# Kernel optimization log

Hardware: AMD Instinct MI355X
Metric: run time of the kernel (lower is better)

Reference implementation:

```python
import jax, jax.numpy as jnp
import numpy as np

B, S, H = 1, 1024, 2048
NH, NKV, HD = 16, 4, 128          # attention heads, kv heads, head_dim
NKUV, E, F = 4, 8, 256            # ffn kuv heads, experts, experts_dim
TOPK = 2
EPS = 1e-6
SCALE = HD ** -0.5


def setup_inputs():
    key = jax.random.key(0)
    ks = jax.random.split(key, 10)
    rn = lambda k, shp, s=0.02: jax.random.normal(k, shp, jnp.float32) * s
    hidden_states = jax.random.normal(ks[0], (B, S, H), jnp.float32)
    # real RoPE tables (base 10000)
    inv = 1.0 / (10000.0 ** (jnp.arange(0, HD, 2, dtype=jnp.float32) / HD))
    freqs = jnp.arange(S, dtype=jnp.float32)[:, None] * inv[None, :]
    emb = jnp.concatenate([freqs, freqs], axis=-1)          # (S, HD)
    cos = jnp.broadcast_to(jnp.cos(emb), (B, S, HD))
    sin = jnp.broadcast_to(jnp.sin(emb), (B, S, HD))
    # additive causal mask
    causal = jnp.tril(jnp.ones((S, S), bool))
    attn_mask = jnp.where(causal, 0.0, -1e9).astype(jnp.float32)[None, None]
    return dict(
        hidden_states=hidden_states, cos=cos, sin=sin, attn_mask=attn_mask,
        ln1_w=jnp.ones((H,), jnp.float32), ln2_w=jnp.ones((H,), jnp.float32),
        wq=rn(ks[1], (NH * HD, H)), wk=rn(ks[2], (NKV * HD, H)),
        wv=rn(ks[3], (NKV * HD, H)), wo=rn(ks[4], (H, NH * HD)),
        mh_norm_w=jnp.ones((NH, HD), jnp.float32),
        router_w=rn(ks[5], (NH, E, HD)),
        k_w=rn(ks[6], (NKUV, E, F, HD)), u_w=rn(ks[7], (NKUV, E, F, HD)),
        v_w=rn(ks[8], (NKUV, E, F, HD)),
    )


def _rmsnorm(x, w, eps=EPS):
    xf = x.astype(jnp.float32)
    var = jnp.mean(xf * xf, axis=-1, keepdims=True)
    return (xf * jax.lax.rsqrt(var + eps) * w).astype(x.dtype)


def _rotate_half(x):
    x1, x2 = jnp.split(x, 2, axis=-1)
    return jnp.concatenate([-x2, x1], axis=-1)


def reference(hidden_states, cos, sin, attn_mask, ln1_w, ln2_w,
              wq, wk, wv, wo, mh_norm_w, router_w, k_w, u_w, v_w):
    # ---- attention block (pre-norm + GQA + RoPE) ----
    x = _rmsnorm(hidden_states, ln1_w)
    q = (x @ wq.T).reshape(B, S, NH, HD).transpose(0, 2, 1, 3)    # (B,NH,S,HD)
    k = (x @ wk.T).reshape(B, S, NKV, HD).transpose(0, 2, 1, 3)   # (B,NKV,S,HD)
    v = (x @ wv.T).reshape(B, S, NKV, HD).transpose(0, 2, 1, 3)
    c, s = cos[:, None], sin[:, None]                              # unsqueeze_dim=1
    q = q * c + _rotate_half(q) * s
    k = k * c + _rotate_half(k) * s
    rep = NH // NKV
    k = jnp.repeat(k, rep, axis=1)                                 # repeat_kv
    v = jnp.repeat(v, rep, axis=1)
    scores = jnp.einsum('bhqd,bhkd->bhqk', q, k) * SCALE + attn_mask
    probs = jax.nn.softmax(scores.astype(jnp.float32), axis=-1).astype(q.dtype)
    attn = jnp.einsum('bhqk,bhkd->bqhd', probs, v).reshape(B, S, NH * HD)
    h = hidden_states + attn @ wo.T
    # ---- multi-head MoE FFN block ----
    y = _rmsnorm(h, ln2_w).reshape(B, S, NH, HD)
    y = _rmsnorm(y, mh_norm_w)                                     # per-head norm
    logits = jnp.einsum('bsnd,ned->bsne', y, router_w)
    rp = jax.nn.softmax(logits.astype(jnp.float32), axis=-1)
    topv, topi = jax.lax.top_k(rp, TOPK)                           # (B,S,NH,TOPK)
    topv = topv / jnp.sum(topv, axis=-1, keepdims=True)
    w_dense = jnp.sum(jax.nn.one_hot(topi, E, dtype=jnp.float32) * topv[..., None],
                      axis=-2).astype(y.dtype)                     # (B,S,NH,E)
    reph = NH // NKUV
    kf = jnp.repeat(k_w, reph, axis=0)                             # repeat_kuv -> (NH,E,F,HD)
    uf = jnp.repeat(u_w, reph, axis=0)
    vf = jnp.repeat(v_w, reph, axis=0)
    gate = jnp.einsum('bsnd,nefd->bsnef', y, kf)
    up = jnp.einsum('bsnd,nefd->bsnef', y, uf)
    act = jax.nn.silu(gate) * up * w_dense[..., None]              # sparse combine weights
    ffn = jnp.einsum('bsnef,nefd->bsnd', act, vf).reshape(B, S, H)
    return h + ffn
```

## Files before the change

### kernel.cpp

```cpp
#include <hip/hip_runtime.h>
#include <hip/hip_bf16.h>

#define S_ 1024
#define H_ 2048
#define NH_ 16
#define NKV_ 4
#define HD_ 128
#define E_ 8
#define F_ 256
#define EPS_ 1e-6f
#define SCALE_ 0.08838834764831845f

typedef __attribute__((ext_vector_type(8))) short bf16x8;
typedef __attribute__((ext_vector_type(4))) float f32x4;

static __device__ __forceinline__ unsigned short f2bf(float x) {
  unsigned u = __float_as_uint(x);
  unsigned r = (u + 0x7FFFu + ((u >> 16) & 1u)) >> 16;
  return (unsigned short)r;
}
static __device__ __forceinline__ float bf2f(unsigned short b) {
  return __uint_as_float(((unsigned)b) << 16);
}
static __device__ __forceinline__ unsigned short f2bh(float x) {
  __hip_bfloat16 b = __float2bfloat16(x);
  return *reinterpret_cast<unsigned short*>(&b);
}

__global__ void rmsnorm1_kernel(const float* __restrict__ in, const float* __restrict__ w,
                                float* __restrict__ out) {
  int s = blockIdx.x, tid = threadIdx.x;
  const float* row = in + s * H_;
  __shared__ float red[256];
  float ss = 0.f;
  for (int i = tid; i < H_; i += 256) { float v = row[i]; ss += v * v; }
  red[tid] = ss; __syncthreads();
  for (int off = 128; off > 0; off >>= 1) {
    if (tid < off) red[tid] += red[tid + off];
    __syncthreads();
  }
  float rs = rsqrtf(red[0] / H_ + EPS_);
  for (int i = tid; i < H_; i += 256) out[s * H_ + i] = row[i] * rs * w[i];
}

__global__ __launch_bounds__(256) void convert_kuw_kernel(const float* __restrict__ kw,
                                                          const float* __restrict__ uw,
                                                          unsigned short* __restrict__ kwb,
                                                          unsigned short* __restrict__ uwb) {
  const float* src = (blockIdx.y == 0) ? kw : uw;
  unsigned short* dst = (blockIdx.y == 0) ? kwb : uwb;
  size_t i = ((size_t)blockIdx.x * 256 + threadIdx.x) * 8;
  float4 a = *(const float4*)&src[i];
  float4 b = *(const float4*)&src[i + 4];
  ushort4 ua, ub;
  ua.x = f2bh(a.x); ua.y = f2bh(a.y); ua.z = f2bh(a.z); ua.w = f2bh(a.w);
  ub.x = f2bh(b.x); ub.y = f2bh(b.y); ub.z = f2bh(b.z); ub.w = f2bh(b.w);
  *(ushort4*)&dst[i] = ua;
  *(ushort4*)&dst[i + 4] = ub;
}

__global__ __launch_bounds__(256) void transpose_vw_kernel(const float* __restrict__ vw,
                                                           unsigned short* __restrict__ vwtb) {
  int e = blockIdx.x, ft = blockIdx.y, dt = blockIdx.z;
  int tid = threadIdx.x;
  __shared__ float tile[64][65];
  const float* src = vw + ((size_t)e * 256 + ft * 64) * 128 + dt * 64;
#pragma unroll
  for (int it = 0; it < 4; ++it) {
    int idx = it * 256 + tid;
    int r = idx >> 4, c4 = (idx & 15) * 4;
    float4 v = *(const float4*)&src[(size_t)r * 128 + c4];
    tile[r][c4] = v.x; tile[r][c4 + 1] = v.y; tile[r][c4 + 2] = v.z; tile[r][c4 + 3] = v.w;
  }
  __syncthreads();
  unsigned short* dst = vwtb + ((size_t)e * 128 + dt * 64) * 256 + ft * 64;
#pragma unroll
  for (int it = 0; it < 4; ++it) {
    int idx = it * 256 + tid;
    int dl = idx >> 4, f4 = (idx & 15) * 4;
    ushort4 u;
    u.x = f2bh(tile[f4 + 0][dl]); u.y = f2bh(tile[f4 + 1][dl]);
    u.z = f2bh(tile[f4 + 2][dl]); u.w = f2bh(tile[f4 + 3][dl]);
    *(ushort4*)&dst[(size_t)dl * 256 + f4] = u;
  }
}

__global__ __launch_bounds__(256) void qkv_mfma_kernel(const float* __restrict__ A,
                                                       const float* __restrict__ wq,
                                                       const float* __restrict__ wk,
                                                       const float* __restrict__ wv,
                                                       float* __restrict__ qb,
                                                       float* __restrict__ kb,
                                                       float* __restrict__ vb) {
  int bm = blockIdx.y * 128;
  int bn = blockIdx.x * 128;
  const float* B; float* C; int ldc, cb;
  if (bn < 2048)      { B = wq + (size_t)bn * 2048;          C = qb; ldc = 2048; cb = bn; }
  else if (bn < 2560) { B = wk + (size_t)(bn - 2048) * 2048; C = kb; ldc = 512;  cb = bn - 2048; }
  else                { B = wv + (size_t)(bn - 2560) * 2048; C = vb; ldc = 512;  cb = bn - 2560; }
  int tid = threadIdx.x, wave = tid >> 6, lane = tid & 63;
  int lq = lane & 15, lg4 = lane >> 4;
  int wr = (wave >> 1) * 64, wc = (wave & 1) * 64;
  __shared__ __align__(16) unsigned short Als[128 * 64];
  __shared__ __align__(16) unsigned short Bls[128 * 64];
  f32x4 acc[4][4];
#pragma unroll
  for (int i = 0; i < 4; ++i)
#pragma unroll
    for (int j = 0; j < 4; ++j) acc[i][j] = (f32x4){0.f, 0.f, 0.f, 0.f};
  for (int k0 = 0; k0 < 2048; k0 += 64) {
    __syncthreads();
#pragma unroll
    for (int it = 0; it < 8; ++it) {
      int idx = it * 256 + tid;
      int r = idx >> 4, c4 = (idx & 15) * 4;
      float4 av = *(const float4*)&A[(size_t)(bm + r) * 2048 + k0 + c4];
      ushort4 ua; ua.x = f2bh(av.x); ua.y = f2bh(av.y); ua.z = f2bh(av.z); ua.w = f2bh(av.w);
      *(ushort4*)((char*)Als + ((r * 128 + c4 * 2) ^ ((r & 7) << 4))) = ua;
      float4 bv = *(const float4*)&B[(size_t)r * 2048 + k0 + c4];
      ushort4 ub; ub.x = f2bh(bv.x); ub.y = f2bh(bv.y); ub.z = f2bh(bv.z); ub.w = f2bh(bv.w);
      *(ushort4*)((char*)Bls + ((r * 128 + c4 * 2) ^ ((r & 7) << 4))) = ub;
    }
    __syncthreads();
#pragma unroll
    for (int ks = 0; ks < 2; ++ks) {
      bf16x8 af[4], bfr[4];
#pragma unroll
      for (int mi = 0; mi < 4; ++mi) {
        int row = wr + mi * 16 + lq;
        af[mi] = *(const bf16x8*)((const char*)Als + ((row * 128 + ks * 64 + lg4 * 16) ^ ((row & 7) << 4)));
      }
#pragma unroll
      for (int ni = 0; ni < 4; ++ni) {
        int row = wc + ni * 16 + lq;
        bfr[ni] = *(const bf16x8*)((const char*)Bls + ((row * 128 + ks * 64 + lg4 * 16) ^ ((row & 7) << 4)));
      }
#pragma unroll
      for (int mi = 0; mi < 4; ++mi)
#pragma unroll
        for (int ni = 0; ni < 4; ++ni)
          acc[mi][ni] = __builtin_amdgcn_mfma_f32_16x16x32_bf16(af[mi], bfr[ni], acc[mi][ni], 0, 0, 0);
    }
  }
#pragma unroll
  for (int mi = 0; mi < 4; ++mi)
#pragma unroll
    for (int ni = 0; ni < 4; ++ni) {
      int col = cb + wc + ni * 16 + lq;
#pragma unroll
      for (int reg = 0; reg < 4; ++reg) {
        int m = bm + wr + mi * 16 + lg4 * 4 + reg;
        C[(size_t)m * ldc + col] = acc[mi][ni][reg];
      }
    }
}

__global__ __launch_bounds__(256) void wo_mfma_kernel(const float* __restrict__ A,
                                                      const float* __restrict__ Bmat,
                                                      const float* __restrict__ resid,
                                                      float* __restrict__ C) {
  int bm = blockIdx.y * 128;
  int bn = blockIdx.x * 128;
  int tid = threadIdx.x, wave = tid >> 6, lane = tid & 63;
  int lq = lane & 15, lg4 = lane >> 4;
  int wr = (wave >> 1) * 64, wc = (wave & 1) * 64;
  __shared__ __align__(16) unsigned short Als[128 * 64];
  __shared__ __align__(16) unsigned short Bls[128 * 64];
  f32x4 acc[4][4];
#pragma unroll
  for (int i = 0; i < 4; ++i)
#pragma unroll
    for (int j = 0; j < 4; ++j) acc[i][j] = (f32x4){0.f, 0.f, 0.f, 0.f};
  for (int k0 = 0; k0 < 2048; k0 += 64) {
    __syncthreads();
#pragma unroll
    for (int it = 0; it < 8; ++it) {
      int idx = it * 256 + tid;
      int r = idx >> 4, c4 = (idx & 15) * 4;
      float4 av = *(const float4*)&A[(size_t)(bm + r) * 2048 + k0 + c4];
      ushort4 ua; ua.x = f2bh(av.x); ua.y = f2bh(av.y); ua.z = f2bh(av.z); ua.w = f2bh(av.w);
      *(ushort4*)((char*)Als + ((r * 128 + c4 * 2) ^ ((r & 7) << 4))) = ua;
      float4 bv = *(const float4*)&Bmat[(size_t)(bn + r) * 2048 + k0 + c4];
      ushort4 ub; ub.x = f2bh(bv.x); ub.y = f2bh(bv.y); ub.z = f2bh(bv.z); ub.w = f2bh(bv.w);
      *(ushort4*)((char*)Bls + ((r * 128 + c4 * 2) ^ ((r & 7) << 4))) = ub;
    }
    __syncthreads();
#pragma unroll
    for (int ks = 0; ks < 2; ++ks) {
      bf16x8 af[4], bfr[4];
#pragma unroll
      for (int mi = 0; mi < 4; ++mi) {
        int row = wr + mi * 16 + lq;
        af[mi] = *(const bf16x8*)((const char*)Als + ((row * 128 + ks * 64 + lg4 * 16) ^ ((row & 7) << 4)));
      }
#pragma unroll
      for (int ni = 0; ni < 4; ++ni) {
        int row = wc + ni * 16 + lq;
        bfr[ni] = *(const bf16x8*)((const char*)Bls + ((row * 128 + ks * 64 + lg4 * 16) ^ ((row & 7) << 4)));
      }
#pragma unroll
      for (int mi = 0; mi < 4; ++mi)
#pragma unroll
        for (int ni = 0; ni < 4; ++ni)
          acc[mi][ni] = __builtin_amdgcn_mfma_f32_16x16x32_bf16(af[mi], bfr[ni], acc[mi][ni], 0, 0, 0);
    }
  }
#pragma unroll
  for (int mi = 0; mi < 4; ++mi)
#pragma unroll
    for (int ni = 0; ni < 4; ++ni) {
      int col = bn + wc + ni * 16 + lq;
#pragma unroll
      for (int reg = 0; reg < 4; ++reg) {
        int m = bm + wr + mi * 16 + lg4 * 4 + reg;
        C[(size_t)m * 2048 + col] = acc[mi][ni][reg] + resid[(size_t)m * 2048 + col];
      }
    }
}

__global__ void rope_kernel(float* __restrict__ qb, float* __restrict__ kb,
                            const float* __restrict__ cosb, const float* __restrict__ sinb) {
  int s = blockIdx.x, tid = threadIdx.x;
  for (int idx = tid; idx < (NH_ + NKV_) * 64; idx += 256) {
    int hh = idx >> 6;
    int d = idx & 63;
    float c0 = cosb[s * HD_ + d], s0 = sinb[s * HD_ + d];
    float c1 = cosb[s * HD_ + d + 64], s1 = sinb[s * HD_ + d + 64];
    float* p;
    if (hh < NH_) p = qb + (size_t)s * 2048 + hh * 128;
    else          p = kb + (size_t)s * 512 + (hh - NH_) * 128;
    float a = p[d], b = p[d + 64];
    p[d] = a * c0 - b * s0;
    p[d + 64] = b * c1 + a * s1;
  }
}

__global__ __launch_bounds__(256) void attn_mfma_kernel(const float* __restrict__ qb,
                                                        const float* __restrict__ kb,
                                                        const float* __restrict__ vb,
                                                        float* __restrict__ ob) {
  int n = blockIdx.x, qt = blockIdx.y;
  int g = n >> 2;
  int tid = threadIdx.x;
  int wave = tid >> 6, lane = tid & 63;
  int lq = lane & 15, lg4 = lane >> 4;

  __shared__ __align__(16) unsigned short Kls[64 * 128];
  __shared__ __align__(16) unsigned short Vls[128 * 64];
  __shared__ __align__(16) unsigned short Pls[4][16 * 64];
  __shared__ __align__(16) float corr_ls[4][16];
  __shared__ __align__(16) float lsum_ls[4][16];

  int q0 = qt * 64 + wave * 16;
  bf16x8 qfrag[4];
  {
    const float* qp = qb + (size_t)(q0 + lq) * 2048 + n * 128;
#pragma unroll
    for (int ks = 0; ks < 4; ++ks) {
      float4 a = *(const float4*)&qp[ks * 32 + lg4 * 8];
      float4 b = *(const float4*)&qp[ks * 32 + lg4 * 8 + 4];
      bf16x8 f;
      f[0] = (short)f2bf(a.x); f[1] = (short)f2bf(a.y);
      f[2] = (short)f2bf(a.z); f[3] = (short)f2bf(a.w);
      f[4] = (short)f2bf(b.x); f[5] = (short)f2bf(b.y);
      f[6] = (short)f2bf(b.z); f[7] = (short)f2bf(b.w);
      qfrag[ks] = f;
    }
  }
  f32x4 oacc[8];
#pragma unroll
  for (int i = 0; i < 8; ++i) oacc[i] = (f32x4){0.f, 0.f, 0.f, 0.f};
  float mrow = -1e30f, lrow = 0.f;

  int nt = qt + 1;
  for (int t = 0; t < nt; ++t) {
    int kv0 = t * 64;
    __syncthreads();
#pragma unroll
    for (int it = 0; it < 8; ++it) {
      int idx = it * 256 + tid;
      int r = idx >> 5;
      int c4 = (idx & 31) * 4;
      size_t gbase = (size_t)(kv0 + r) * 512 + g * 128 + c4;
      float4 kv = *(const float4*)&kb[gbase];
      ushort4 u;
      u.x = f2bf(kv.x); u.y = f2bf(kv.y); u.z = f2bf(kv.z); u.w = f2bf(kv.w);
      *(ushort4*)((char*)Kls + ((r * 256 + c4 * 2) ^ ((r & 7) << 4))) = u;
      float4 vv = *(const float4*)&vb[gbase];
      unsigned short vs0 = f2bf(vv.x), vs1 = f2bf(vv.y), vs2 = f2bf(vv.z), vs3 = f2bf(vv.w);
      *(unsigned short*)((char*)Vls + (((c4 + 0) * 128 + r * 2) ^ (((c4 + 0) & 7) << 4))) = vs0;
      *(unsigned short*)((char*)Vls + (((c4 + 1) * 128 + r * 2) ^ (((c4 + 1) & 7) << 4))) = vs1;
      *(unsigned short*)((char*)Vls + (((c4 + 2) * 128 + r * 2) ^ (((c4 + 2) & 7) << 4))) = vs2;
      *(unsigned short*)((char*)Vls + (((c4 + 3) * 128 + r * 2) ^ (((c4 + 3) & 7) << 4))) = vs3;
    }
    __syncthreads();
    f32x4 sacc[4];
#pragma unroll
    for (int i = 0; i < 4; ++i) sacc[i] = (f32x4){0.f, 0.f, 0.f, 0.f};
#pragma unroll
    for (int kt = 0; kt < 4; ++kt) {
      int row = kt * 16 + lq;
#pragma unroll
      for (int ks = 0; ks < 4; ++ks) {
        bf16x8 kf = *(const bf16x8*)((const char*)Kls +
                     ((row * 256 + ks * 64 + lg4 * 16) ^ ((row & 7) << 4)));
        sacc[kt] = __builtin_amdgcn_mfma_f32_16x16x32_bf16(kf, qfrag[ks], sacc[kt], 0, 0, 0);
      }
    }
    int qg = q0 + lq;
    float s[16], p[16];
    float rmax = -1e30f;
#pragma unroll
    for (int kt = 0; kt < 4; ++kt) {
#pragma unroll
      for (int r = 0; r < 4; ++r) {
        int kg = kv0 + kt * 16 + lg4 * 4 + r;
        float v = sacc[kt][r] * SCALE_;
        v = (kg <= qg) ? v : -1e30f;
        s[kt * 4 + r] = v;
        rmax = fmaxf(rmax, v);
      }
    }
    rmax = fmaxf(rmax, __shfl_xor(rmax, 16));
    rmax = fmaxf(rmax, __shfl_xor(rmax, 32));
    float mnew = fmaxf(mrow, rmax);
    float corr = __expf(mrow - mnew);
    float psum = 0.f;
#pragma unroll
    for (int i = 0; i < 16; ++i) { p[i] = __expf(s[i] - mnew); psum += p[i]; }
    psum += __shfl_xor(psum, 16);
    psum += __shfl_xor(psum, 32);
    lrow = lrow * corr + psum;
    mrow = mnew;
    if (lane < 16) corr_ls[wave][lq] = corr;
#pragma unroll
    for (int kt = 0; kt < 4; ++kt) {
      unsigned u0 = (unsigned)f2bf(p[kt * 4 + 0]) | ((unsigned)f2bf(p[kt * 4 + 1]) << 16);
      unsigned u1 = (unsigned)f2bf(p[kt * 4 + 2]) | ((unsigned)f2bf(p[kt * 4 + 3]) << 16);
      int colb = kt * 32 + lg4 * 8;
      *(unsigned*)((char*)&Pls[wave][0] + ((lq * 128 + colb) ^ ((lq & 7) << 4))) = u0;
      *(unsigned*)((char*)&Pls[wave][0] + ((lq * 128 + colb + 4) ^ ((lq & 7) << 4))) = u1;
    }
    f32x4 c4v = *(const f32x4*)&corr_ls[wave][lg4 * 4];
#pragma unroll
    for (int dt = 0; dt < 8; ++dt) {
#pragma unroll
      for (int r = 0; r < 4; ++r) oacc[dt][r] *= c4v[r];
    }
    bf16x8 pfrag[2];
#pragma unroll
    for (int ks2 = 0; ks2 < 2; ++ks2)
      pfrag[ks2] = *(const bf16x8*)((const char*)&Pls[wave][0] +
                    ((lq * 128 + ks2 * 64 + lg4 * 16) ^ ((lq & 7) << 4)));
#pragma unroll
    for (int dt = 0; dt < 8; ++dt) {
      int dr = dt * 16 + lq;
#pragma unroll
      for (int ks2 = 0; ks2 < 2; ++ks2) {
        bf16x8 vf = *(const bf16x8*)((const char*)Vls +
                     ((dr * 128 + ks2 * 64 + lg4 * 16) ^ ((dr & 7) << 4)));
        oacc[dt] = __builtin_amdgcn_mfma_f32_16x16x32_bf16(pfrag[ks2], vf, oacc[dt], 0, 0, 0);
      }
    }
  }
  if (lane < 16) lsum_ls[wave][lq] = lrow;
  f32x4 l4 = *(const f32x4*)&lsum_ls[wave][lg4 * 4];
#pragma unroll
  for (int dt = 0; dt < 8; ++dt) {
#pragma unroll
    for (int r = 0; r < 4; ++r) {
      ob[(size_t)(q0 + lg4 * 4 + r) * 2048 + n * 128 + dt * 16 + lq] = oacc[dt][r] / l4[r];
    }
  }
}

__global__ void rmsnorm2_kernel(const float* __restrict__ hin, const float* __restrict__ ln2w,
                                const float* __restrict__ mhw, float* __restrict__ yout,
                                unsigned short* __restrict__ ybb) {
  int s = blockIdx.x, tid = threadIdx.x;
  const float* row = hin + (size_t)s * H_;
  __shared__ float y1[H_];
  __shared__ float red[256];
  __shared__ float ph[16][17];
  float ss = 0.f;
  for (int i = tid; i < H_; i += 256) { float v = row[i]; ss += v * v; }
  red[tid] = ss; __syncthreads();
  for (int off = 128; off > 0; off >>= 1) {
    if (tid < off) red[tid] += red[tid + off];
    __syncthreads();
  }
  float rs1 = rsqrtf(red[0] / H_ + EPS_);
  for (int i = tid; i < H_; i += 256) y1[i] = row[i] * rs1 * ln2w[i];
  __syncthreads();
  int n = tid >> 4, j = tid & 15;
  float s2 = 0.f;
  for (int d = j * 8; d < j * 8 + 8; ++d) { float v = y1[n * 128 + d]; s2 += v * v; }
  ph[n][j] = s2; __syncthreads();
  if (j == 0) {
    float t = 0.f;
    for (int q = 0; q < 16; ++q) t += ph[n][q];
    ph[n][16] = rsqrtf(t / HD_ + EPS_);
  }
  __syncthreads();
  for (int i = tid; i < H_; i += 256) {
    int hn = i >> 7;
    float v = y1[i] * ph[hn][16] * mhw[i];
    yout[(size_t)s * H_ + i] = v;
    ybb[(size_t)s * H_ + i] = f2bh(v);
  }
}

__global__ void route_kernel(const float* __restrict__ yb, const float* __restrict__ rw,
                             int* __restrict__ cnt, int* __restrict__ idxb,
                             float* __restrict__ wtb) {
  int s = blockIdx.x, tid = threadIdx.x;
  int n = tid >> 3, e = tid & 7;
  const float* yrow = yb + (size_t)s * 2048 + n * 128;
  const float* wrow = rw + (size_t)(n * 8 + e) * 128;
  float lg = 0.f;
  for (int d = 0; d < 128; ++d) lg += yrow[d] * wrow[d];
  float mx = lg;
  for (int off = 1; off < 8; off <<= 1) mx = fmaxf(mx, __shfl_xor(mx, off));
  float p = __expf(lg - mx);
  float sum = p;
  for (int off = 1; off < 8; off <<= 1) sum += __shfl_xor(sum, off);
  float rp = p / sum;
  float v1 = rp; int i1 = e;
  for (int off = 1; off < 8; off <<= 1) {
    float ov = __shfl_xor(v1, off); int oi = __shfl_xor(i1, off);
    if (ov > v1 || (ov == v1 && oi < i1)) { v1 = ov; i1 = oi; }
  }
  float v2 = (e == i1) ? -1e30f : rp; int i2 = e;
  for (int off = 1; off < 8; off <<= 1) {
    float ov = __shfl_xor(v2, off); int oi = __shfl_xor(i2, off);
    if (ov > v2 || (ov == v2 && oi < i2)) { v2 = ov; i2 = oi; }
  }
  if (e == 0) {
    float wsum = v1 + v2;
    int pe1 = n * 8 + i1;
    int pos1 = atomicAdd(&cnt[pe1], 1);
    idxb[pe1 * S_ + pos1] = s; wtb[pe1 * S_ + pos1] = v1 / wsum;
    int pe2 = n * 8 + i2;
    int pos2 = atomicAdd(&cnt[pe2], 1);
    idxb[pe2 * S_ + pos2] = s; wtb[pe2 * S_ + pos2] = v2 / wsum;
  }
}

__global__ __launch_bounds__(256) void moe_ffn_mfma_kernel(
    const unsigned short* __restrict__ ybb, const unsigned short* __restrict__ kwb,
    const unsigned short* __restrict__ uwb, const unsigned short* __restrict__ vwtb,
    const int* __restrict__ cnt, const int* __restrict__ idxb,
    const float* __restrict__ wtb, float* __restrict__ out) {
  int pe = blockIdx.x;
  int c = cnt[pe];
  int base = blockIdx.y * 64;
  if (base >= c) return;
  int n = pe >> 3, e = pe & 7, g = n >> 2;
  int eW = g * 8 + e;
  int nr = min(64, c - base);
  int tid = threadIdx.x, wave = tid >> 6, lane = tid & 63;
  int lq = lane & 15, lg4 = lane >> 4;

  __shared__ __align__(16) unsigned short Yls[64 * 128];
  __shared__ __align__(16) unsigned short WstK[64 * 128];
  __shared__ __align__(16) unsigned short WstU[64 * 128];
  __shared__ __align__(16) unsigned short WstV[128 * 64];
  __shared__ __align__(16) unsigned short Act[4][16 * 64];
  __shared__ int sidx[64];
  __shared__ float swt[64];

  if (tid < 64) {
    sidx[tid] = (tid < nr) ? idxb[pe * S_ + base + tid] : 0;
    swt[tid]  = (tid < nr) ? wtb[pe * S_ + base + tid] : 0.f;
  }
  __syncthreads();
#pragma unroll
  for (int it = 0; it < 4; ++it) {
    int idx = it * 256 + tid;
    int r = idx >> 4, c8 = (idx & 15) * 8;
    bf16x8 v = {0, 0, 0, 0, 0, 0, 0, 0};
    if (r < nr) v = *(const bf16x8*)&ybb[(size_t)sidx[r] * 2048 + n * 128 + c8];
    *(bf16x8*)((char*)Yls + ((r * 256 + c8 * 2) ^ ((r & 7) << 4))) = v;
  }
  __syncthreads();
  bf16x8 yfrag[4];
  {
    int arow = wave * 16 + lq;
#pragma unroll
    for (int ks = 0; ks < 4; ++ks)
      yfrag[ks] = *(const bf16x8*)((const char*)Yls + ((arow * 256 + ks * 64 + lg4 * 16) ^ ((arow & 7) << 4)));
  }
  float wts[4];
#pragma unroll
  for (int reg = 0; reg < 4; ++reg) wts[reg] = swt[wave * 16 + lg4 * 4 + reg];

  f32x4 dacc[8];
#pragma unroll
  for (int i = 0; i < 8; ++i) dacc[i] = (f32x4){0.f, 0.f, 0.f, 0.f};

  for (int fc = 0; fc < 4; ++fc) {
    __syncthreads();
#pragma unroll
    for (int it = 0; it < 4; ++it) {
      int idx = it * 256 + tid;
      int r = idx >> 4, c8 = (idx & 15) * 8;
      size_t goff = ((size_t)(eW * 256 + fc * 64 + r)) * 128 + c8;
      bf16x8 kv = *(const bf16x8*)&kwb[goff];
      *(bf16x8*)((char*)WstK + ((r * 256 + c8 * 2) ^ ((r & 7) << 4))) = kv;
      bf16x8 uv = *(const bf16x8*)&uwb[goff];
      *(bf16x8*)((char*)WstU + ((r * 256 + c8 * 2) ^ ((r & 7) << 4))) = uv;
    }
#pragma unroll
    for (int it = 0; it < 4; ++it) {
      int idx = it * 256 + tid;
      int r = idx >> 3, c8 = (idx & 7) * 8;
      bf16x8 vv = *(const bf16x8*)&vwtb[((size_t)(eW * 128 + r)) * 256 + fc * 64 + c8];
      *(bf16x8*)((char*)WstV + ((r * 128 + c8 * 2) ^ ((r & 7) << 4))) = vv;
    }
    __syncthreads();
    f32x4 gacc[4], uacc[4];
#pragma unroll
    for (int i = 0; i < 4; ++i) { gacc[i] = (f32x4){0.f, 0.f, 0.f, 0.f}; uacc[i] = (f32x4){0.f, 0.f, 0.f, 0.f}; }
#pragma unroll
    for (int ks = 0; ks < 4; ++ks) {
#pragma unroll
      for (int nf = 0; nf < 4; ++nf) {
        int brow = nf * 16 + lq;
        bf16x8 bk = *(const bf16x8*)((const char*)WstK + ((brow * 256 + ks * 64 + lg4 * 16) ^ ((brow & 7) << 4)));
        gacc[nf] = __builtin_amdgcn_mfma_f32_16x16x32_bf16(yfrag[ks], bk, gacc[nf], 0, 0, 0);
        bf16x8 bu = *(const bf16x8*)((const char*)WstU + ((brow * 256 + ks * 64 + lg4 * 16) ^ ((brow & 7) << 4)));
        uacc[nf] = __builtin_amdgcn_mfma_f32_16x16x32_bf16(yfrag[ks], bu, uacc[nf], 0, 0, 0);
      }
    }
#pragma unroll
    for (int nf = 0; nf < 4; ++nf) {
#pragma unroll
      for (int reg = 0; reg < 4; ++reg) {
        int m = lg4 * 4 + reg;
        int f = nf * 16 + lq;
        float gg = gacc[nf][reg];
        float uu = uacc[nf][reg];
        float sig = 1.f / (1.f + __expf(-gg));
        float av = gg * sig * uu * wts[reg];
        *(unsigned short*)((char*)&Act[wave][0] + ((m * 128 + f * 2) ^ ((m & 7) << 4))) = f2bh(av);
      }
    }
    bf16x8 afrag[2];
#pragma unroll
    for (int ks2 = 0; ks2 < 2; ++ks2)
      afrag[ks2] = *(const bf16x8*)((const char*)&Act[wave][0] + ((lq * 128 + ks2 * 64 + lg4 * 16) ^ ((lq & 7) << 4)));
#pragma unroll
    for (int nd = 0; nd < 8; ++nd) {
      int drow = nd * 16 + lq;
#pragma unroll
      for (int ks2 = 0; ks2 < 2; ++ks2) {
        bf16x8 b = *(const bf16x8*)((const char*)WstV + ((drow * 128 + ks2 * 64 + lg4 * 16) ^ ((drow & 7) << 4)));
        dacc[nd] = __builtin_amdgcn_mfma_f32_16x16x32_bf16(afrag[ks2], b, dacc[nd], 0, 0, 0);
      }
    }
  }
#pragma unroll
  for (int nd = 0; nd < 8; ++nd) {
    int d = nd * 16 + lq;
#pragma unroll
    for (int reg = 0; reg < 4; ++reg) {
      int mloc = wave * 16 + lg4 * 4 + reg;
      if (mloc < nr) {
        atomicAdd(&out[(size_t)sidx[mloc] * 2048 + n * 128 + d], dacc[nd][reg]);
      }
    }
  }
}

extern "C" void kernel_launch(void* const* d_in, const int* in_sizes, int n_in,
                              void* d_out, int out_size, void* d_ws, size_t ws_size,
                              hipStream_t stream) {
  const float* hidden = (const float*)d_in[0];
  const float* cosb   = (const float*)d_in[1];
  const float* sinb   = (const float*)d_in[2];
  const float* ln1w   = (const float*)d_in[4];
  const float* ln2w   = (const float*)d_in[5];
  const float* wq     = (const float*)d_in[6];
  const float* wk     = (const float*)d_in[7];
  const float* wv     = (const float*)d_in[8];
  const float* wo     = (const float*)d_in[9];
  const float* mhw    = (const float*)d_in[10];
  const float* rw     = (const float*)d_in[11];
  const float* kww    = (const float*)d_in[12];
  const float* uww    = (const float*)d_in[13];
  const float* vww    = (const float*)d_in[14];
  float* out = (float*)d_out;

  float* ws = (float*)d_ws;
  float* x     = ws;
  float* qb    = x + 2097152;
  float* kb    = qb + 2097152;
  float* vb    = kb + 524288;
  float* attnb = vb + 524288;
  float* yb    = attnb + 2097152;
  int*   cntb  = (int*)(yb + 2097152);
  int*   idxb  = cntb + 128;
  float* wtb   = (float*)(idxb + 131072);
  unsigned short* ybb  = (unsigned short*)(wtb + 131072);
  unsigned short* kwb  = ybb + 2097152;
  unsigned short* uwb  = kwb + 1048576;
  unsigned short* vwtb = uwb + 1048576;

  hipMemsetAsync(cntb, 0, 128 * sizeof(int), stream);

  convert_kuw_kernel<<<dim3(512, 2), 256, 0, stream>>>(kww, uww, kwb, uwb);
  transpose_vw_kernel<<<dim3(32, 4, 2), 256, 0, stream>>>(vww, vwtb);

  rmsnorm1_kernel<<<S_, 256, 0, stream>>>(hidden, ln1w, x);

  qkv_mfma_kernel<<<dim3(24, 8), 256, 0, stream>>>(x, wq, wk, wv, qb, kb, vb);

  rope_kernel<<<S_, 256, 0, stream>>>(qb, kb, cosb, sinb);

  attn_mfma_kernel<<<dim3(NH_, S_ / 64), 256, 0, stream>>>(qb, kb, vb, attnb);

  wo_mfma_kernel<<<dim3(16, 8), 256, 0, stream>>>(attnb, wo, hidden, out);

  rmsnorm2_kernel<<<S_, 256, 0, stream>>>(out, ln2w, mhw, yb, ybb);

  route_kernel<<<S_, 128, 0, stream>>>(yb, rw, cntb, idxb, wtb);

  moe_ffn_mfma_kernel<<<dim3(128, 16), 256, 0, stream>>>(ybb, kwb, uwb, vwtb, cntb, idxb, wtb, out);
}
```

Baseline: 437.7 us.

## Store intermediates in bf16 and double-buffer QKV/WO GEMMs with smaller tiles

The normalized input, V, the roped Q/K and the attention output are now written as bf16 instead of fp32, which halves their memory traffic and removes repeated conversions in the consumer kernels. The QKV and output-projection GEMMs switch to 64x128 tiles with a swizzled 1D grid, so more blocks run and neighbouring blocks share data in cache. They also use a register-staged double buffer that overlaps global loads with MFMA work. The attention K/V staging uses wider 16-byte loads. Rounding happens earlier in the pipeline, though operands were already converted to bf16 before the MFMAs.

```diff
diff --git a/kernel.cpp b/kernel.cpp
--- a/kernel.cpp
+++ b/kernel.cpp
@@ -19,16 +19,13 @@
   unsigned r = (u + 0x7FFFu + ((u >> 16) & 1u)) >> 16;
   return (unsigned short)r;
 }
-static __device__ __forceinline__ float bf2f(unsigned short b) {
-  return __uint_as_float(((unsigned)b) << 16);
-}
 static __device__ __forceinline__ unsigned short f2bh(float x) {
   __hip_bfloat16 b = __float2bfloat16(x);
   return *reinterpret_cast<unsigned short*>(&b);
 }
 
 __global__ void rmsnorm1_kernel(const float* __restrict__ in, const float* __restrict__ w,
-                                float* __restrict__ out) {
+                                unsigned short* __restrict__ outb) {
   int s = blockIdx.x, tid = threadIdx.x;
   const float* row = in + s * H_;
   __shared__ float red[256];
@@ -40,7 +37,7 @@
     __syncthreads();
   }
   float rs = rsqrtf(red[0] / H_ + EPS_);
-  for (int i = tid; i < H_; i += 256) out[s * H_ + i] = row[i] * rs * w[i];
+  for (int i = tid; i < H_; i += 256) outb[(size_t)s * H_ + i] = f2bh(row[i] * rs * w[i]);
 }
 
 __global__ __launch_bounds__(256) void convert_kuw_kernel(const float* __restrict__ kw,
@@ -85,128 +82,179 @@
   }
 }
 
-__global__ __launch_bounds__(256) void qkv_mfma_kernel(const float* __restrict__ A,
+__global__ __launch_bounds__(256) void qkv_mfma_kernel(const unsigned short* __restrict__ xb,
                                                        const float* __restrict__ wq,
                                                        const float* __restrict__ wk,
                                                        const float* __restrict__ wv,
                                                        float* __restrict__ qb,
                                                        float* __restrict__ kb,
-                                                       float* __restrict__ vb) {
-  int bm = blockIdx.y * 128;
-  int bn = blockIdx.x * 128;
-  const float* B; float* C; int ldc, cb;
+                                                       unsigned short* __restrict__ vbb) {
+  int bid = blockIdx.x;
+  int swz = (bid & 7) * 48 + (bid >> 3);
+  int bm = (swz / 24) * 64;
+  int bn = (swz % 24) * 128;
+  const float* B; float* C = nullptr; unsigned short* Cb = nullptr; int ldc, cb;
   if (bn < 2048)      { B = wq + (size_t)bn * 2048;          C = qb; ldc = 2048; cb = bn; }
   else if (bn < 2560) { B = wk + (size_t)(bn - 2048) * 2048; C = kb; ldc = 512;  cb = bn - 2048; }
-  else                { B = wv + (size_t)(bn - 2560) * 2048; C = vb; ldc = 512;  cb = bn - 2560; }
+  else                { B = wv + (size_t)(bn - 2560) * 2048; Cb = vbb; ldc = 512; cb = bn - 2560; }
   int tid = threadIdx.x, wave = tid >> 6, lane = tid & 63;
   int lq = lane & 15, lg4 = lane >> 4;
-  int wr = (wave >> 1) * 64, wc = (wave & 1) * 64;
-  __shared__ __align__(16) unsigned short Als[128 * 64];
-  __shared__ __align__(16) unsigned short Bls[128 * 64];
-  f32x4 acc[4][4];
-#pragma unroll
-  for (int i = 0; i < 4; ++i)
+  int wr = (wave >> 1) * 32, wc = (wave & 1) * 64;
+  __shared__ __align__(16) unsigned short Als[2][64 * 64];
+  __shared__ __align__(16) unsigned short Bls[2][128 * 64];
+  f32x4 acc[2][4];
+#pragma unroll
+  for (int i = 0; i < 2; ++i)
 #pragma unroll
     for (int j = 0; j < 4; ++j) acc[i][j] = (f32x4){0.f, 0.f, 0.f, 0.f};
-  for (int k0 = 0; k0 < 2048; k0 += 64) {
-    __syncthreads();
+
+  int ar = (tid >> 3), ac8 = (tid & 7) * 8;
+  int br = (tid >> 4), bc4 = (tid & 15) * 4;
+  bf16x8 areg[2];
+  float4 breg[8];
+
+  auto LOAD = [&](int k0) {
+#pragma unroll
+    for (int it = 0; it < 2; ++it)
+      areg[it] = *(const bf16x8*)&xb[(size_t)(bm + ar + it * 32) * 2048 + k0 + ac8];
+#pragma unroll
+    for (int it = 0; it < 8; ++it)
+      breg[it] = *(const float4*)&B[(size_t)(br + it * 16) * 2048 + k0 + bc4];
+  };
+  auto STORE = [&](int buf) {
+#pragma unroll
+    for (int it = 0; it < 2; ++it) {
+      int r = ar + it * 32;
+      *(bf16x8*)((char*)&Als[buf][0] + ((r * 128 + ac8 * 2) ^ ((r & 7) << 4))) = areg[it];
+    }
 #pragma unroll
     for (int it = 0; it < 8; ++it) {
-      int idx = it * 256 + tid;
-      int r = idx >> 4, c4 = (idx & 15) * 4;
-      float4 av = *(const float4*)&A[(size_t)(bm + r) * 2048 + k0 + c4];
-      ushort4 ua; ua.x = f2bh(av.x); ua.y = f2bh(av.y); ua.z = f2bh(av.z); ua.w = f2bh(av.w);
-      *(ushort4*)((char*)Als + ((r * 128 + c4 * 2) ^ ((r & 7) << 4))) = ua;
-      float4 bv = *(const float4*)&B[(size_t)r * 2048 + k0 + c4];
-      ushort4 ub; ub.x = f2bh(bv.x); ub.y = f2bh(bv.y); ub.z = f2bh(bv.z); ub.w = f2bh(bv.w);
-      *(ushort4*)((char*)Bls + ((r * 128 + c4 * 2) ^ ((r & 7) << 4))) = ub;
-    }
-    __syncthreads();
+      int r = br + it * 16;
+      ushort4 u;
+      u.x = f2bh(breg[it].x); u.y = f2bh(breg[it].y);
+      u.z = f2bh(breg[it].z); u.w = f2bh(breg[it].w);
+      *(ushort4*)((char*)&Bls[buf][0] + ((r * 128 + bc4 * 2) ^ ((r & 7) << 4))) = u;
+    }
+  };
+
+  LOAD(0); STORE(0); __syncthreads();
+  int cur = 0;
+  for (int t = 0; t < 32; ++t) {
+    if (t < 31) LOAD((t + 1) * 64);
 #pragma unroll
     for (int ks = 0; ks < 2; ++ks) {
-      bf16x8 af[4], bfr[4];
-#pragma unroll
-      for (int mi = 0; mi < 4; ++mi) {
+      bf16x8 af[2], bfr[4];
+#pragma unroll
+      for (int mi = 0; mi < 2; ++mi) {
         int row = wr + mi * 16 + lq;
-        af[mi] = *(const bf16x8*)((const char*)Als + ((row * 128 + ks * 64 + lg4 * 16) ^ ((row & 7) << 4)));
+        af[mi] = *(const bf16x8*)((const char*)&Als[cur][0] + ((row * 128 + ks * 64 + lg4 * 16) ^ ((row & 7) << 4)));
       }
 #pragma unroll
       for (int ni = 0; ni < 4; ++ni) {
         int row = wc + ni * 16 + lq;
-        bfr[ni] = *(const bf16x8*)((const char*)Bls + ((row * 128 + ks * 64 + lg4 * 16) ^ ((row & 7) << 4)));
-      }
-#pragma unroll
-      for (int mi = 0; mi < 4; ++mi)
+        bfr[ni] = *(const bf16x8*)((const char*)&Bls[cur][0] + ((row * 128 + ks * 64 + lg4 * 16) ^ ((row & 7) << 4)));
+      }
+#pragma unroll
+      for (int mi = 0; mi < 2; ++mi)
 #pragma unroll
         for (int ni = 0; ni < 4; ++ni)
           acc[mi][ni] = __builtin_amdgcn_mfma_f32_16x16x32_bf16(af[mi], bfr[ni], acc[mi][ni], 0, 0, 0);
     }
-  }
-#pragma unroll
-  for (int mi = 0; mi < 4; ++mi)
+    if (t < 31) STORE(cur ^ 1);
+    __syncthreads();
+    cur ^= 1;
+  }
+#pragma unroll
+  for (int mi = 0; mi < 2; ++mi)
 #pragma unroll
     for (int ni = 0; ni < 4; ++ni) {
       int col = cb + wc + ni * 16 + lq;
 #pragma unroll
       for (int reg = 0; reg < 4; ++reg) {
         int m = bm + wr + mi * 16 + lg4 * 4 + reg;
-        C[(size_t)m * ldc + col] = acc[mi][ni][reg];
-      }
-    }
-}
-
-__global__ __launch_bounds__(256) void wo_mfma_kernel(const float* __restrict__ A,
+        if (C) C[(size_t)m * ldc + col] = acc[mi][ni][reg];
+        else   Cb[(size_t)m * ldc + col] = f2bh(acc[mi][ni][reg]);
+      }
+    }
+}
+
+__global__ __launch_bounds__(256) void wo_mfma_kernel(const unsigned short* __restrict__ A,
                                                       const float* __restrict__ Bmat,
                                                       const float* __restrict__ resid,
                                                       float* __restrict__ C) {
-  int bm = blockIdx.y * 128;
-  int bn = blockIdx.x * 128;
+  int bid = blockIdx.x;
+  int swz = (bid & 7) * 32 + (bid >> 3);
+  int bm = (swz / 16) * 64;
+  int bn = (swz % 16) * 128;
   int tid = threadIdx.x, wave = tid >> 6, lane = tid & 63;
   int lq = lane & 15, lg4 = lane >> 4;
-  int wr = (wave >> 1) * 64, wc = (wave & 1) * 64;
-  __shared__ __align__(16) unsigned short Als[128 * 64];
-  __shared__ __align__(16) unsigned short Bls[128 * 64];
-  f32x4 acc[4][4];
-#pragma unroll
-  for (int i = 0; i < 4; ++i)
+  int wr = (wave >> 1) * 32, wc = (wave & 1) * 64;
+  __shared__ __align__(16) unsigned short Als[2][64 * 64];
+  __shared__ __align__(16) unsigned short Bls[2][128 * 64];
+  f32x4 acc[2][4];
+#pragma unroll
+  for (int i = 0; i < 2; ++i)
 #pragma unroll
     for (int j = 0; j < 4; ++j) acc[i][j] = (f32x4){0.f, 0.f, 0.f, 0.f};
-  for (int k0 = 0; k0 < 2048; k0 += 64) {
-    __syncthreads();
+
+  int ar = (tid >> 3), ac8 = (tid & 7) * 8;
+  int br = (tid >> 4), bc4 = (tid & 15) * 4;
+  bf16x8 areg[2];
+  float4 breg[8];
+
+  auto LOAD = [&](int k0) {
+#pragma unroll
+    for (int it = 0; it < 2; ++it)
+      areg[it] = *(const bf16x8*)&A[(size_t)(bm + ar + it * 32) * 2048 + k0 + ac8];
+#pragma unroll
+    for (int it = 0; it < 8; ++it)
+      breg[it] = *(const float4*)&Bmat[(size_t)(bn + br + it * 16) * 2048 + k0 + bc4];
+  };
+  auto STORE = [&](int buf) {
+#pragma unroll
+    for (int it = 0; it < 2; ++it) {
+      int r = ar + it * 32;
+      *(bf16x8*)((char*)&Als[buf][0] + ((r * 128 + ac8 * 2) ^ ((r & 7) << 4))) = areg[it];
+    }
 #pragma unroll
     for (int it = 0; it < 8; ++it) {
-      int idx = it * 256 + tid;
-      int r = idx >> 4, c4 = (idx & 15) * 4;
-      float4 av = *(const float4*)&A[(size_t)(bm + r) * 2048 + k0 + c4];
-      ushort4 ua; ua.x = f2bh(av.x); ua.y = f2bh(av.y); ua.z = f2bh(av.z); ua.w = f2bh(av.w);
-      *(ushort4*)((char*)Als + ((r * 128 + c4 * 2) ^ ((r & 7) << 4))) = ua;
-      float4 bv = *(const float4*)&Bmat[(size_t)(bn + r) * 2048 + k0 + c4];
-      ushort4 ub; ub.x = f2bh(bv.x); ub.y = f2bh(bv.y); ub.z = f2bh(bv.z); ub.w = f2bh(bv.w);
-      *(ushort4*)((char*)Bls + ((r * 128 + c4 * 2) ^ ((r & 7) << 4))) = ub;
-    }
-    __syncthreads();
+      int r = br + it * 16;
+      ushort4 u;
+      u.x = f2bh(breg[it].x); u.y = f2bh(breg[it].y);
+      u.z = f2bh(breg[it].z); u.w = f2bh(breg[it].w);
+      *(ushort4*)((char*)&Bls[buf][0] + ((r * 128 + bc4 * 2) ^ ((r & 7) << 4))) = u;
+    }
+  };
+
+  LOAD(0); STORE(0); __syncthreads();
+  int cur = 0;
+  for (int t = 0; t < 32; ++t) {
+    if (t < 31) LOAD((t + 1) * 64);
 #pragma unroll
     for (int ks = 0; ks < 2; ++ks) {
-      bf16x8 af[4], bfr[4];
-#pragma unroll
-      for (int mi = 0; mi < 4; ++mi) {
+      bf16x8 af[2], bfr[4];
+#pragma unroll
+      for (int mi = 0; mi < 2; ++mi) {
         int row = wr + mi * 16 + lq;
-        af[mi] = *(const bf16x8*)((const char*)Als + ((row * 128 + ks * 64 + lg4 * 16) ^ ((row & 7) << 4)));
+        af[mi] = *(const bf16x8*)((const char*)&Als[cur][0] + ((row * 128 + ks * 64 + lg4 * 16) ^ ((row & 7) << 4)));
       }
 #pragma unroll
       for (int ni = 0; ni < 4; ++ni) {
         int row = wc + ni * 16 + lq;
-        bfr[ni] = *(const bf16x8*)((const char*)Bls + ((row * 128 + ks * 64 + lg4 * 16) ^ ((row & 7) << 4)));
-      }
-#pragma unroll
-      for (int mi = 0; mi < 4; ++mi)
+        bfr[ni] = *(const bf16x8*)((const char*)&Bls[cur][0] + ((row * 128 + ks * 64 + lg4 * 16) ^ ((row & 7) << 4)));
+      }
+#pragma unroll
+      for (int mi = 0; mi < 2; ++mi)
 #pragma unroll
         for (int ni = 0; ni < 4; ++ni)
           acc[mi][ni] = __builtin_amdgcn_mfma_f32_16x16x32_bf16(af[mi], bfr[ni], acc[mi][ni], 0, 0, 0);
     }
-  }
-#pragma unroll
-  for (int mi = 0; mi < 4; ++mi)
+    if (t < 31) STORE(cur ^ 1);
+    __syncthreads();
+    cur ^= 1;
+  }
+#pragma unroll
+  for (int mi = 0; mi < 2; ++mi)
 #pragma unroll
     for (int ni = 0; ni < 4; ++ni) {
       int col = bn + wc + ni * 16 + lq;
@@ -218,27 +266,28 @@
     }
 }
 
-__global__ void rope_kernel(float* __restrict__ qb, float* __restrict__ kb,
-                            const float* __restrict__ cosb, const float* __restrict__ sinb) {
+__global__ void rope_kernel(const float* __restrict__ qb, const float* __restrict__ kb,
+                            const float* __restrict__ cosb, const float* __restrict__ sinb,
+                            unsigned short* __restrict__ qbb, unsigned short* __restrict__ kbb) {
   int s = blockIdx.x, tid = threadIdx.x;
   for (int idx = tid; idx < (NH_ + NKV_) * 64; idx += 256) {
     int hh = idx >> 6;
     int d = idx & 63;
     float c0 = cosb[s * HD_ + d], s0 = sinb[s * HD_ + d];
     float c1 = cosb[s * HD_ + d + 64], s1 = sinb[s * HD_ + d + 64];
-    float* p;
-    if (hh < NH_) p = qb + (size_t)s * 2048 + hh * 128;
-    else          p = kb + (size_t)s * 512 + (hh - NH_) * 128;
-    float a = p[d], b = p[d + 64];
-    p[d] = a * c0 - b * s0;
-    p[d + 64] = b * c1 + a * s1;
-  }
-}
-
-__global__ __launch_bounds__(256) void attn_mfma_kernel(const float* __restrict__ qb,
-                                                        const float* __restrict__ kb,
-                                                        const float* __restrict__ vb,
-                                                        float* __restrict__ ob) {
+    const float* src; unsigned short* dst;
+    if (hh < NH_) { src = qb + (size_t)s * 2048 + hh * 128; dst = qbb + (size_t)s * 2048 + hh * 128; }
+    else          { src = kb + (size_t)s * 512 + (hh - NH_) * 128; dst = kbb + (size_t)s * 512 + (hh - NH_) * 128; }
+    float a = src[d], b = src[d + 64];
+    dst[d] = f2bh(a * c0 - b * s0);
+    dst[d + 64] = f2bh(b * c1 + a * s1);
+  }
+}
+
+__global__ __launch_bounds__(256) void attn_mfma_kernel(const unsigned short* __restrict__ qbb,
+                                                        const unsigned short* __restrict__ kbb,
+                                                        const unsigned short* __restrict__ vbb,
+                                                        unsigned short* __restrict__ ob) {
   int n = blockIdx.x, qt = blockIdx.y;
   int g = n >> 2;
   int tid = threadIdx.x;
@@ -254,18 +303,10 @@
   int q0 = qt * 64 + wave * 16;
   bf16x8 qfrag[4];
   {
-    const float* qp = qb + (size_t)(q0 + lq) * 2048 + n * 128;
-#pragma unroll
-    for (int ks = 0; ks < 4; ++ks) {
-      float4 a = *(const float4*)&qp[ks * 32 + lg4 * 8];
-      float4 b = *(const float4*)&qp[ks * 32 + lg4 * 8 + 4];
-      bf16x8 f;
-      f[0] = (short)f2bf(a.x); f[1] = (short)f2bf(a.y);
-      f[2] = (short)f2bf(a.z); f[3] = (short)f2bf(a.w);
-      f[4] = (short)f2bf(b.x); f[5] = (short)f2bf(b.y);
-      f[6] = (short)f2bf(b.z); f[7] = (short)f2bf(b.w);
-      qfrag[ks] = f;
-    }
+    const unsigned short* qp = qbb + (size_t)(q0 + lq) * 2048 + n * 128;
+#pragma unroll
+    for (int ks = 0; ks < 4; ++ks)
+      qfrag[ks] = *(const bf16x8*)&qp[ks * 32 + lg4 * 8];
   }
   f32x4 oacc[8];
 #pragma unroll
@@ -277,21 +318,18 @@
     int kv0 = t * 64;
     __syncthreads();
 #pragma unroll
-    for (int it = 0; it < 8; ++it) {
+    for (int it = 0; it < 4; ++it) {
       int idx = it * 256 + tid;
-      int r = idx >> 5;
-      int c4 = (idx & 31) * 4;
-      size_t gbase = (size_t)(kv0 + r) * 512 + g * 128 + c4;
-      float4 kv = *(const float4*)&kb[gbase];
-      ushort4 u;
-      u.x = f2bf(kv.x); u.y = f2bf(kv.y); u.z = f2bf(kv.z); u.w = f2bf(kv.w);
-      *(ushort4*)((char*)Kls + ((r * 256 + c4 * 2) ^ ((r & 7) << 4))) = u;
-      float4 vv = *(const float4*)&vb[gbase];
-      unsigned short vs0 = f2bf(vv.x), vs1 = f2bf(vv.y), vs2 = f2bf(vv.z), vs3 = f2bf(vv.w);
-      *(unsigned short*)((char*)Vls + (((c4 + 0) * 128 + r * 2) ^ (((c4 + 0) & 7) << 4))) = vs0;
-      *(unsigned short*)((char*)Vls + (((c4 + 1) * 128 + r * 2) ^ (((c4 + 1) & 7) << 4))) = vs1;
-      *(unsigned short*)((char*)Vls + (((c4 + 2) * 128 + r * 2) ^ (((c4 + 2) & 7) << 4))) = vs2;
-      *(unsigned short*)((char*)Vls + (((c4 + 3) * 128 + r * 2) ^ (((c4 + 3) & 7) << 4))) = vs3;
+      int r = idx >> 4, c8 = (idx & 15) * 8;
+      size_t gbase = (size_t)(kv0 + r) * 512 + g * 128 + c8;
+      bf16x8 kv = *(const bf16x8*)&kbb[gbase];
+      *(bf16x8*)((char*)Kls + ((r * 256 + c8 * 2) ^ ((r & 7) << 4))) = kv;
+      bf16x8 vv = *(const bf16x8*)&vbb[gbase];
+#pragma unroll
+      for (int j = 0; j < 8; ++j) {
+        int d = c8 + j;
+        *(unsigned short*)((char*)Vls + ((d * 128 + r * 2) ^ ((j) << 4))) = (unsigned short)vv[j];
+      }
     }
     __syncthreads();
     f32x4 sacc[4];
@@ -369,7 +407,7 @@
   for (int dt = 0; dt < 8; ++dt) {
 #pragma unroll
     for (int r = 0; r < 4; ++r) {
-      ob[(size_t)(q0 + lg4 * 4 + r) * 2048 + n * 128 + dt * 16 + lq] = oacc[dt][r] / l4[r];
+      ob[(size_t)(q0 + lg4 * 4 + r) * 2048 + n * 128 + dt * 16 + lq] = f2bh(oacc[dt][r] / l4[r]);
     }
   }
 }
@@ -592,34 +630,36 @@
   float* out = (float*)d_out;
 
   float* ws = (float*)d_ws;
-  float* x     = ws;
-  float* qb    = x + 2097152;
+  float* qb    = ws;
   float* kb    = qb + 2097152;
-  float* vb    = kb + 524288;
-  float* attnb = vb + 524288;
-  float* yb    = attnb + 2097152;
+  float* yb    = kb + 524288;
   int*   cntb  = (int*)(yb + 2097152);
   int*   idxb  = cntb + 128;
   float* wtb   = (float*)(idxb + 131072);
-  unsigned short* ybb  = (unsigned short*)(wtb + 131072);
-  unsigned short* kwb  = ybb + 2097152;
-  unsigned short* uwb  = kwb + 1048576;
-  unsigned short* vwtb = uwb + 1048576;
+  unsigned short* xb    = (unsigned short*)(wtb + 131072);
+  unsigned short* qbb   = xb + 2097152;
+  unsigned short* kbb   = qbb + 2097152;
+  unsigned short* vbb   = kbb + 524288;
+  unsigned short* attnbb= vbb + 524288;
+  unsigned short* ybb   = attnbb + 2097152;
+  unsigned short* kwb   = ybb + 2097152;
+  unsigned short* uwb   = kwb + 1048576;
+  unsigned short* vwtb  = uwb + 1048576;
 
   hipMemsetAsync(cntb, 0, 128 * sizeof(int), stream);
 
   convert_kuw_kernel<<<dim3(512, 2), 256, 0, stream>>>(kww, uww, kwb, uwb);
   transpose_vw_kernel<<<dim3(32, 4, 2), 256, 0, stream>>>(vww, vwtb);
 
-  rmsnorm1_kernel<<<S_, 256, 0, stream>>>(hidden, ln1w, x);
-
-  qkv_mfma_kernel<<<dim3(24, 8), 256, 0, stream>>>(x, wq, wk, wv, qb, kb, vb);
-
-  rope_kernel<<<S_, 256, 0, stream>>>(qb, kb, cosb, sinb);
-
-  attn_mfma_kernel<<<dim3(NH_, S_ / 64), 256, 0, stream>>>(qb, kb, vb, attnb);
-
-  wo_mfma_kernel<<<dim3(16, 8), 256, 0, stream>>>(attnb, wo, hidden, out);
+  rmsnorm1_kernel<<<S_, 256, 0, stream>>>(hidden, ln1w, xb);
+
+  qkv_mfma_kernel<<<384, 256, 0, stream>>>(xb, wq, wk, wv, qb, kb, vbb);
+
+  rope_kernel<<<S_, 256, 0, stream>>>(qb, kb, cosb, sinb, qbb, kbb);
+
+  attn_mfma_kernel<<<dim3(NH_, S_ / 64), 256, 0, stream>>>(qbb, kbb, vbb, attnbb);
+
+  wo_mfma_kernel<<<256, 256, 0, stream>>>(attnbb, wo, hidden, out);
 
   rmsnorm2_kernel<<<S_, 256, 0, stream>>>(out, ln2w, mhw, yb, ybb);
 
```

Result: faster. 378.3 us (-13.6%).
